# Performance work log

Measured on AMD Instinct MI355X. Metric: run time of the kernel, lower is better.

## Reference

```python
import jax, jax.numpy as jnp
import numpy as np

N = 100000      # num nodes
E = 1600000     # num edges
F_IN = 602      # Reddit input features
H = 256         # num_hidden
C = 42          # num_classes


def gcn_conv(x, src, dst, W, b, num_nodes):
    """PyG GCNConv: add self loops, symmetric deg^-1/2 normalization, scatter-add."""
    h = x @ W  # [N, out] dense transform first (PyG order)
    self_idx = jnp.arange(num_nodes, dtype=src.dtype)
    s = jnp.concatenate([src, self_idx])  # [E+N]
    d = jnp.concatenate([dst, self_idx])
    deg = jax.ops.segment_sum(jnp.ones_like(d, dtype=h.dtype), d, num_segments=num_nodes)
    dinv = deg ** -0.5  # deg >= 1 due to self loops
    norm = dinv[s] * dinv[d]  # [E+N]
    msg = h[s] * norm[:, None]  # [E+N, out] gather + scale
    out = jax.ops.segment_sum(msg, d, num_segments=num_nodes)  # scatter-add
    return out + b


def setup_inputs() -> dict:
    key = jax.random.key(0)
    k = jax.random.split(key, 5)
    x = jax.random.normal(k[0], (N, F_IN), dtype=jnp.float32)
    edge_index = jax.random.randint(k[1], (2, E), 0, N, dtype=jnp.int32)
    # Glorot-style init for GCNConv linear weights; bias zeros (PyG default)
    W1 = jax.random.normal(k[2], (F_IN, H), dtype=jnp.float32) * np.float32(1.0 / np.sqrt(F_IN))
    b1 = jnp.zeros((H,), dtype=jnp.float32)
    W2 = jax.random.normal(k[3], (H, C), dtype=jnp.float32) * np.float32(1.0 / np.sqrt(H))
    b2 = jnp.zeros((C,), dtype=jnp.float32)
    return {"x": x, "edge_index": edge_index, "W1": W1, "b1": b1, "W2": W2, "b2": b2}


def reference(x, edge_index, W1, b1, W2, b2):
    src, dst = edge_index[0], edge_index[1]
    num_nodes = x.shape[0]
    h = gcn_conv(x, src, dst, W1, b1, num_nodes)
    h = jax.nn.relu(h)
    # dropout is identity in eval mode (deterministic reference)
    out = gcn_conv(h, src, dst, W2, b2, num_nodes)
    return jax.nn.log_softmax(out, axis=1)
```

## Files before the change

kernel.cpp:

```cpp
#include <hip/hip_runtime.h>
#include <stdint.h>

#define NN 100000
#define NE 1600000
#define FIN 602
#define KP1 608
#define H 256
#define C 42
#define NP2 48
#define NB1 98

typedef __bf16 bf16;
typedef __bf16 bf16x8 __attribute__((ext_vector_type(8)));
typedef float f32x4 __attribute__((ext_vector_type(4)));

__device__ __forceinline__ float b2f(bf16 v) { return (float)v; }
__device__ __forceinline__ bf16 f2b(float v) { return (bf16)v; }
__device__ __forceinline__ float us2f(unsigned short u) {
    union { unsigned int i; float f; } w; w.i = ((unsigned int)u) << 16; return w.f;
}


__global__ void k_zero(int* __restrict__ p, int n) {
    int i = blockIdx.x * 256 + threadIdx.x;
    if (i < n) p[i] = 0;
}

__global__ void k_count(const int* __restrict__ dst, int* __restrict__ cnt) {
    int e = blockIdx.x * 256 + threadIdx.x;
    if (e < NE) atomicAdd(&cnt[dst[e]], 1);
}

__global__ void k_dinv(const int* __restrict__ cnt, float* __restrict__ dinv) {
    int i = blockIdx.x * 256 + threadIdx.x;
    if (i < NN) dinv[i] = rsqrtf((float)(cnt[i] + 1));
}

__global__ __launch_bounds__(256) void k_scan1(const int* __restrict__ cnt,
                                               int* __restrict__ excl, int* __restrict__ bsum) {
    __shared__ int ts[256];
    const int tid = threadIdx.x;
    const int base = blockIdx.x * 1024 + tid * 4;
    int v[4];
#pragma unroll
    for (int j = 0; j < 4; ++j) v[j] = (base + j < NN) ? cnt[base + j] : 0;
    int s = v[0] + v[1] + v[2] + v[3];
    ts[tid] = s;
    __syncthreads();
    for (int off = 1; off < 256; off <<= 1) {
        int t = (tid >= off) ? ts[tid - off] : 0;
        __syncthreads();
        if (tid >= off) ts[tid] += t;
        __syncthreads();
    }
    int prefix = ts[tid] - s;
    if (tid == 255) bsum[blockIdx.x] = ts[255];
    int run = prefix;
#pragma unroll
    for (int j = 0; j < 4; ++j) {
        if (base + j < NN) excl[base + j] = run;
        run += v[j];
    }
}

__global__ __launch_bounds__(128) void k_scan2(int* __restrict__ bsum) {
    __shared__ int ts[128];
    const int tid = threadIdx.x;
    int v = (tid < NB1) ? bsum[tid] : 0;
    ts[tid] = v;
    __syncthreads();
    for (int off = 1; off < 128; off <<= 1) {
        int t = (tid >= off) ? ts[tid - off] : 0;
        __syncthreads();
        if (tid >= off) ts[tid] += t;
        __syncthreads();
    }
    if (tid < NB1) bsum[tid] = ts[tid] - v;
}

__global__ __launch_bounds__(256) void k_scan3(const int* __restrict__ excl, const int* __restrict__ bsum,
                                               int* __restrict__ rowptr, int* __restrict__ cursor) {
    const int tid = threadIdx.x;
    const int base = blockIdx.x * 1024 + tid * 4;
    const int add = bsum[blockIdx.x];
#pragma unroll
    for (int j = 0; j < 4; ++j) {
        int i = base + j;
        if (i < NN) { int r = excl[i] + add; rowptr[i] = r; cursor[i] = r; }
    }
    if (blockIdx.x == 0 && tid == 0) rowptr[NN] = NE;
}

__global__ void k_fill(const int* __restrict__ src, const int* __restrict__ dst,
                       int* __restrict__ cursor, int* __restrict__ esrc) {
    int e = blockIdx.x * 256 + threadIdx.x;
    if (e < NE) {
        int d = dst[e];
        int pos = atomicAdd(&cursor[d], 1);
        esrc[pos] = src[e];
    }
}


__global__ void k_transpose_w1(const float* __restrict__ w1, bf16* __restrict__ w1t) {
    int idx = blockIdx.x * 256 + threadIdx.x;
    int n = idx / KP1;
    int k = idx % KP1;
    w1t[idx] = (k < FIN) ? f2b(w1[(size_t)k * H + n]) : (bf16)0.0f;
}

__global__ void k_transpose_w2(const float* __restrict__ w2, bf16* __restrict__ w2t) {
    int idx = blockIdx.x * 256 + threadIdx.x;
    int n = idx >> 8;
    int k = idx & 255;
    w2t[idx] = (n < C) ? f2b(w2[(size_t)k * C + n]) : (bf16)0.0f;
}


__global__ __launch_bounds__(256) void k_gemm1(const float* __restrict__ x,
                                               const bf16* __restrict__ w1t,
                                               bf16* __restrict__ h1) {
    const int tid = threadIdx.x;
    const int wave = tid >> 6;
    const int lane = tid & 63;
    const int q = lane >> 4;
    const int r = lane & 15;
    const int b = blockIdx.x;
    const int row0 = (b >> 1) * 64;
    const int col0 = (b & 1) * 128 + wave * 32;

    const float* arow[4];
#pragma unroll
    for (int rt = 0; rt < 4; ++rt) {
        int m = row0 + rt * 16 + r;
        if (m >= NN) m = NN - 1;
        arow[rt] = x + (size_t)m * FIN + q * 8;
    }
    const bf16* brow[2];
#pragma unroll
    for (int ct = 0; ct < 2; ++ct)
        brow[ct] = w1t + (size_t)(col0 + ct * 16 + r) * KP1 + q * 8;

    f32x4 acc[4][2];
#pragma unroll
    for (int a = 0; a < 4; ++a)
#pragma unroll
        for (int c = 0; c < 2; ++c) acc[a][c] = (f32x4){0.f, 0.f, 0.f, 0.f};

#pragma unroll 2
    for (int kk = 0; kk < 18; ++kk) {
        const int k0 = kk * 32;
        bf16x8 af[4];
#pragma unroll
        for (int rt = 0; rt < 4; ++rt) {
            const float2* p = (const float2*)(arow[rt] + k0);
            float2 f0 = p[0], f1 = p[1], f2 = p[2], f3 = p[3];
            union { bf16 s[8]; bf16x8 v; } pk;
            pk.s[0] = f2b(f0.x); pk.s[1] = f2b(f0.y);
            pk.s[2] = f2b(f1.x); pk.s[3] = f2b(f1.y);
            pk.s[4] = f2b(f2.x); pk.s[5] = f2b(f2.y);
            pk.s[6] = f2b(f3.x); pk.s[7] = f2b(f3.y);
            af[rt] = pk.v;
        }
#pragma unroll
        for (int ct = 0; ct < 2; ++ct) {
            union { uint4 u; bf16x8 v; } ub;
            ub.u = *(const uint4*)(brow[ct] + k0);
#pragma unroll
            for (int rt = 0; rt < 4; ++rt)
                acc[rt][ct] = __builtin_amdgcn_mfma_f32_16x16x32_bf16(af[rt], ub.v, acc[rt][ct], 0, 0, 0);
        }
    }

    {
        const int k0 = 576;
        bf16x8 af[4];
#pragma unroll
        for (int rt = 0; rt < 4; ++rt) {
            union { bf16 s[8]; bf16x8 v; } pk;
            if (q < 3) {
                const float2* p = (const float2*)(arow[rt] + k0);
                float2 f0 = p[0], f1 = p[1], f2 = p[2], f3 = p[3];
                pk.s[0] = f2b(f0.x); pk.s[1] = f2b(f0.y);
                pk.s[2] = f2b(f1.x); pk.s[3] = f2b(f1.y);
                pk.s[4] = f2b(f2.x); pk.s[5] = f2b(f2.y);
                pk.s[6] = f2b(f3.x); pk.s[7] = f2b(f3.y);
            } else {
                const float* p = arow[rt] + k0;
                pk.s[0] = f2b(p[0]); pk.s[1] = f2b(p[1]);
#pragma unroll
                for (int j = 2; j < 8; ++j) pk.s[j] = (bf16)0.0f;
            }
            af[rt] = pk.v;
        }
#pragma unroll
        for (int ct = 0; ct < 2; ++ct) {
            union { uint4 u; bf16x8 v; } ub;
            ub.u = *(const uint4*)(brow[ct] + k0);
#pragma unroll
            for (int rt = 0; rt < 4; ++rt)
                acc[rt][ct] = __builtin_amdgcn_mfma_f32_16x16x32_bf16(af[rt], ub.v, acc[rt][ct], 0, 0, 0);
        }
    }

#pragma unroll
    for (int rt = 0; rt < 4; ++rt) {
#pragma unroll
        for (int ct = 0; ct < 2; ++ct) {
            const int col = col0 + ct * 16 + r;
#pragma unroll
            for (int rr = 0; rr < 4; ++rr) {
                const int m = row0 + rt * 16 + q * 4 + rr;
                if (m < NN) h1[(size_t)m * H + col] = f2b(acc[rt][ct][rr]);
            }
        }
    }
}


__global__ __launch_bounds__(64) void k_gather1(const int* __restrict__ rowptr,
                                                const int* __restrict__ esrc,
                                                const bf16* __restrict__ h1,
                                                const float* __restrict__ dinv,
                                                const float* __restrict__ b1,
                                                bf16* __restrict__ hb) {
    const int n = blockIdx.x;
    const int tid = threadIdx.x;
    const float dn = dinv[n];

    uint2 u = ((const uint2*)(h1 + (size_t)n * H))[tid];
    float ws = dn * dn;
    float a0 = us2f((unsigned short)(u.x & 0xffff)) * ws;
    float a1 = us2f((unsigned short)(u.x >> 16)) * ws;
    float a2 = us2f((unsigned short)(u.y & 0xffff)) * ws;
    float a3 = us2f((unsigned short)(u.y >> 16)) * ws;

    const int beg = rowptr[n], end = rowptr[n + 1];
    int j = beg;
    for (; j + 3 < end; j += 4) {
        int s0 = esrc[j], s1 = esrc[j + 1], s2 = esrc[j + 2], s3 = esrc[j + 3];
        float w0 = dinv[s0] * dn, w1 = dinv[s1] * dn, w2 = dinv[s2] * dn, w3 = dinv[s3] * dn;
        uint2 v0 = ((const uint2*)(h1 + (size_t)s0 * H))[tid];
        uint2 v1 = ((const uint2*)(h1 + (size_t)s1 * H))[tid];
        uint2 v2 = ((const uint2*)(h1 + (size_t)s2 * H))[tid];
        uint2 v3 = ((const uint2*)(h1 + (size_t)s3 * H))[tid];
        a0 += us2f((unsigned short)(v0.x & 0xffff)) * w0;
        a1 += us2f((unsigned short)(v0.x >> 16)) * w0;
        a2 += us2f((unsigned short)(v0.y & 0xffff)) * w0;
        a3 += us2f((unsigned short)(v0.y >> 16)) * w0;
        a0 += us2f((unsigned short)(v1.x & 0xffff)) * w1;
        a1 += us2f((unsigned short)(v1.x >> 16)) * w1;
        a2 += us2f((unsigned short)(v1.y & 0xffff)) * w1;
        a3 += us2f((unsigned short)(v1.y >> 16)) * w1;
        a0 += us2f((unsigned short)(v2.x & 0xffff)) * w2;
        a1 += us2f((unsigned short)(v2.x >> 16)) * w2;
        a2 += us2f((unsigned short)(v2.y & 0xffff)) * w2;
        a3 += us2f((unsigned short)(v2.y >> 16)) * w2;
        a0 += us2f((unsigned short)(v3.x & 0xffff)) * w3;
        a1 += us2f((unsigned short)(v3.x >> 16)) * w3;
        a2 += us2f((unsigned short)(v3.y & 0xffff)) * w3;
        a3 += us2f((unsigned short)(v3.y >> 16)) * w3;
    }
    for (; j < end; ++j) {
        int s = esrc[j];
        float w = dinv[s] * dn;
        uint2 v = ((const uint2*)(h1 + (size_t)s * H))[tid];
        a0 += us2f((unsigned short)(v.x & 0xffff)) * w;
        a1 += us2f((unsigned short)(v.x >> 16)) * w;
        a2 += us2f((unsigned short)(v.y & 0xffff)) * w;
        a3 += us2f((unsigned short)(v.y >> 16)) * w;
    }

    float4 bb = ((const float4*)b1)[tid];
    a0 += bb.x; a1 += bb.y; a2 += bb.z; a3 += bb.w;
    a0 = a0 > 0.f ? a0 : 0.f;
    a1 = a1 > 0.f ? a1 : 0.f;
    a2 = a2 > 0.f ? a2 : 0.f;
    a3 = a3 > 0.f ? a3 : 0.f;

    union { unsigned short s[4]; uint2 u; } pk;
    union { bf16 b; unsigned short s; } cv;
    cv.b = f2b(a0); pk.s[0] = cv.s;
    cv.b = f2b(a1); pk.s[1] = cv.s;
    cv.b = f2b(a2); pk.s[2] = cv.s;
    cv.b = f2b(a3); pk.s[3] = cv.s;
    ((uint2*)(hb + (size_t)n * H))[tid] = pk.u;
}


__global__ __launch_bounds__(256) void k_gemm2(const bf16* __restrict__ hb,
                                               const bf16* __restrict__ w2t,
                                               bf16* __restrict__ h2) {
    const int tid = threadIdx.x;
    const int wave = tid >> 6;
    const int lane = tid & 63;
    const int q = lane >> 4;
    const int r = lane & 15;
    const int row0 = blockIdx.x * 128 + wave * 32;

    const bf16* arow[2];
#pragma unroll
    for (int rt = 0; rt < 2; ++rt) {
        int m = row0 + rt * 16 + r;
        if (m >= NN) m = NN - 1;
        arow[rt] = hb + (size_t)m * H + q * 8;
    }
    const bf16* brow[3];
#pragma unroll
    for (int ct = 0; ct < 3; ++ct)
        brow[ct] = w2t + (size_t)(ct * 16 + r) * H + q * 8;

    f32x4 acc[2][3];
#pragma unroll
    for (int a = 0; a < 2; ++a)
#pragma unroll
        for (int c = 0; c < 3; ++c) acc[a][c] = (f32x4){0.f, 0.f, 0.f, 0.f};

#pragma unroll 2
    for (int kk = 0; kk < 8; ++kk) {
        const int k0 = kk * 32;
        bf16x8 af[2];
#pragma unroll
        for (int rt = 0; rt < 2; ++rt) {
            union { uint4 u; bf16x8 v; } ua;
            ua.u = *(const uint4*)(arow[rt] + k0);
            af[rt] = ua.v;
        }
#pragma unroll
        for (int ct = 0; ct < 3; ++ct) {
            union { uint4 u; bf16x8 v; } ub;
            ub.u = *(const uint4*)(brow[ct] + k0);
#pragma unroll
            for (int rt = 0; rt < 2; ++rt)
                acc[rt][ct] = __builtin_amdgcn_mfma_f32_16x16x32_bf16(af[rt], ub.v, acc[rt][ct], 0, 0, 0);
        }
    }

#pragma unroll
    for (int rt = 0; rt < 2; ++rt) {
#pragma unroll
        for (int ct = 0; ct < 3; ++ct) {
            const int col = ct * 16 + r;
            if (col < C) {
#pragma unroll
                for (int rr = 0; rr < 4; ++rr) {
                    const int m = row0 + rt * 16 + q * 4 + rr;
                    if (m < NN) h2[(size_t)m * C + col] = f2b(acc[rt][ct][rr]);
                }
            }
        }
    }
}


__global__ __launch_bounds__(64) void k_gather2(const int* __restrict__ rowptr,
                                                const int* __restrict__ esrc,
                                                const bf16* __restrict__ h2,
                                                const float* __restrict__ dinv,
                                                const float* __restrict__ b2,
                                                float* __restrict__ out) {
    const int n = blockIdx.x;
    const int c = threadIdx.x;
    const float dn = dinv[n];

    float acc = 0.f;
    if (c < C) acc = b2f(h2[(size_t)n * C + c]) * dn * dn;

    const int beg = rowptr[n], end = rowptr[n + 1];
    int j = beg;
    for (; j + 3 < end; j += 4) {
        int s0 = esrc[j], s1 = esrc[j + 1], s2 = esrc[j + 2], s3 = esrc[j + 3];
        float w0 = dinv[s0] * dn, w1 = dinv[s1] * dn, w2 = dinv[s2] * dn, w3 = dinv[s3] * dn;
        if (c < C) {
            float v0 = b2f(h2[(size_t)s0 * C + c]);
            float v1 = b2f(h2[(size_t)s1 * C + c]);
            float v2 = b2f(h2[(size_t)s2 * C + c]);
            float v3 = b2f(h2[(size_t)s3 * C + c]);
            acc += v0 * w0 + v1 * w1 + v2 * w2 + v3 * w3;
        }
    }
    for (; j < end; ++j) {
        int s = esrc[j];
        float w = dinv[s] * dn;
        if (c < C) acc += b2f(h2[(size_t)s * C + c]) * w;
    }

    float v = (c < C) ? acc + b2[c] : -INFINITY;
    float m = v;
#pragma unroll
    for (int o = 32; o > 0; o >>= 1) m = fmaxf(m, __shfl_xor(m, o, 64));
    float ex = (c < C) ? expf(v - m) : 0.f;
    float s = ex;
#pragma unroll
    for (int o = 32; o > 0; o >>= 1) s += __shfl_xor(s, o, 64);
    if (c < C) out[(size_t)n * C + c] = (v - m) - logf(s);
}


extern "C" void kernel_launch(void* const* d_in, const int* in_sizes, int n_in,
                              void* d_out, int out_size, void* d_ws, size_t ws_size,
                              hipStream_t stream) {
    const float* x  = (const float*)d_in[0];
    const int*   ei = (const int*)d_in[1];
    const float* w1 = (const float*)d_in[2];
    const float* b1 = (const float*)d_in[3];
    const float* w2 = (const float*)d_in[4];
    const float* b2 = (const float*)d_in[5];
    float* out = (float*)d_out;

    const int* src = ei;
    const int* dst = ei + NE;

    char* base = (char*)d_ws;
    size_t off = 0;
    auto alloc = [&](size_t bytes) -> void* {
        void* p = base + off;
        off += (bytes + 255) & ~(size_t)255;
        return p;
    };
    int*   cnt    = (int*)alloc((size_t)NN * 4);
    float* dinv   = (float*)alloc((size_t)NN * 4);
    int*   excl   = (int*)alloc((size_t)NN * 4);
    int*   bsum   = (int*)alloc(128 * 4);
    int*   rowptr = (int*)alloc((size_t)(NN + 1) * 4);
    int*   cursor = (int*)alloc((size_t)NN * 4);
    int*   esrc   = (int*)alloc((size_t)NE * 4);
    bf16*  w1t    = (bf16*)alloc((size_t)H * KP1 * 2);
    bf16*  w2t    = (bf16*)alloc((size_t)NP2 * H * 2);
    bf16*  h1     = (bf16*)alloc((size_t)NN * H * 2);
    bf16*  hb     = (bf16*)alloc((size_t)NN * H * 2);
    bf16*  h2     = (bf16*)alloc((size_t)NN * C * 2);
    (void)ws_size;

    k_zero<<<dim3((NN + 255) / 256), dim3(256), 0, stream>>>(cnt, NN);
    k_count<<<dim3((NE + 255) / 256), dim3(256), 0, stream>>>(dst, cnt);
    k_dinv<<<dim3((NN + 255) / 256), dim3(256), 0, stream>>>(cnt, dinv);
    k_scan1<<<dim3(NB1), dim3(256), 0, stream>>>(cnt, excl, bsum);
    k_scan2<<<dim3(1), dim3(128), 0, stream>>>(bsum);
    k_scan3<<<dim3(NB1), dim3(256), 0, stream>>>(excl, bsum, rowptr, cursor);
    k_fill<<<dim3((NE + 255) / 256), dim3(256), 0, stream>>>(src, dst, cursor, esrc);

    k_transpose_w1<<<dim3(KP1), dim3(256), 0, stream>>>(w1, w1t);
    k_transpose_w2<<<dim3(NP2), dim3(256), 0, stream>>>(w2, w2t);

    k_gemm1<<<dim3(2 * ((NN + 63) / 64)), dim3(256), 0, stream>>>(x, w1t, h1);
    k_gather1<<<dim3(NN), dim3(64), 0, stream>>>(rowptr, esrc, h1, dinv, b1, hb);

    k_gemm2<<<dim3((NN + 127) / 128), dim3(256), 0, stream>>>(hb, w2t, h2);
    k_gather2<<<dim3(NN), dim3(64), 0, stream>>>(rowptr, esrc, h2, dinv, b2, out);
}
```

Baseline: 944.3 us.

## Pre-convert x to padded bf16 and pipeline GEMM1 through LDS

A separate kernel first converts the fp32 input features into a padded bf16 buffer. GEMM1 then covers 128 rows by all 256 columns per 512-thread block, streaming A tiles into a triple-buffered, XOR-swizzled LDS ring with direct global-to-LDS loads. Each block now reads x once instead of twice, and the wider per-wave tile means more reuse of each loaded fragment. The cost is an extra pass that writes and re-reads the bf16 copy, and the workspace for hb/h2 is aliased onto the xb buffer.

```diff
diff --git a/kernel.cpp b/kernel.cpp
--- a/kernel.cpp
+++ b/kernel.cpp
@@ -9,6 +9,8 @@
 #define C 42
 #define NP2 48
 #define NB1 98
+#define KBLK 32
+#define NCH (NN * 76)
 
 typedef __bf16 bf16;
 typedef __bf16 bf16x8 __attribute__((ext_vector_type(8)));
@@ -117,100 +119,119 @@
 }
 
 
-__global__ __launch_bounds__(256) void k_gemm1(const float* __restrict__ x,
-                                               const bf16* __restrict__ w1t,
-                                               bf16* __restrict__ h1) {
+__global__ __launch_bounds__(256) void k_convert(const float* __restrict__ x,
+                                                 bf16* __restrict__ xb) {
+    int idx = blockIdx.x * 256 + threadIdx.x;
+    if (idx >= NCH) return;
+    int n = idx / 76;
+    int rem = idx - n * 76;
+    int c0 = rem * 8;
+    const float* p = x + (size_t)n * FIN + c0;
+    union { bf16 s[8]; uint4 u; } pk;
+    if (c0 + 8 <= FIN) {
+        float2 f0 = ((const float2*)p)[0];
+        float2 f1 = ((const float2*)p)[1];
+        float2 f2v = ((const float2*)p)[2];
+        float2 f3 = ((const float2*)p)[3];
+        pk.s[0] = f2b(f0.x);  pk.s[1] = f2b(f0.y);
+        pk.s[2] = f2b(f1.x);  pk.s[3] = f2b(f1.y);
+        pk.s[4] = f2b(f2v.x); pk.s[5] = f2b(f2v.y);
+        pk.s[6] = f2b(f3.x);  pk.s[7] = f2b(f3.y);
+    } else {
+#pragma unroll
+        for (int j = 0; j < 8; ++j)
+            pk.s[j] = (c0 + j < FIN) ? f2b(p[j]) : (bf16)0.0f;
+    }
+    *(uint4*)(xb + (size_t)n * KP1 + c0) = pk.u;
+}
+
+
+__global__ __launch_bounds__(512, 4) void k_gemm1(const bf16* __restrict__ xb,
+                                                  const bf16* __restrict__ w1t,
+                                                  bf16* __restrict__ h1) {
+    __shared__ bf16 As[3 * 128 * KBLK];
     const int tid = threadIdx.x;
     const int wave = tid >> 6;
     const int lane = tid & 63;
     const int q = lane >> 4;
     const int r = lane & 15;
-    const int b = blockIdx.x;
-    const int row0 = (b >> 1) * 64;
-    const int col0 = (b & 1) * 128 + wave * 32;
-
-    const float* arow[4];
+    const int row0 = blockIdx.x * 128;
+    const int wrow0 = (wave & 1) * 64;
+    const int wcol0 = (wave >> 1) * 64;
+
+    const int sg = (tid & 3) ^ ((tid >> 2) & 3) ^ ((tid >> 4) & 3);
+    int gsrow = row0 + (tid >> 2);
+    if (gsrow >= NN) gsrow = NN - 1;
+    const bf16* gsrc = xb + (size_t)gsrow * KP1 + sg * 8;
+
+    int aoff[4];
 #pragma unroll
     for (int rt = 0; rt < 4; ++rt) {
-        int m = row0 + rt * 16 + r;
-        if (m >= NN) m = NN - 1;
-        arow[rt] = x + (size_t)m * FIN + q * 8;
-    }
-    const bf16* brow[2];
-#pragma unroll
-    for (int ct = 0; ct < 2; ++ct)
-        brow[ct] = w1t + (size_t)(col0 + ct * 16 + r) * KP1 + q * 8;
-
-    f32x4 acc[4][2];
+        int R = wrow0 + rt * 16 + r;
+        int gq = q ^ (R & 3) ^ ((R >> 2) & 3);
+        aoff[rt] = R * KBLK + gq * 8;
+    }
+
+    const bf16* brow[4];
+#pragma unroll
+    for (int ct = 0; ct < 4; ++ct)
+        brow[ct] = w1t + (size_t)(wcol0 + ct * 16 + r) * KP1 + q * 8;
+
+    f32x4 acc[4][4];
 #pragma unroll
     for (int a = 0; a < 4; ++a)
 #pragma unroll
-        for (int c = 0; c < 2; ++c) acc[a][c] = (f32x4){0.f, 0.f, 0.f, 0.f};
-
-#pragma unroll 2
-    for (int kk = 0; kk < 18; ++kk) {
-        const int k0 = kk * 32;
+        for (int b = 0; b < 4; ++b) acc[a][b] = (f32x4){0.f, 0.f, 0.f, 0.f};
+
+    auto stage = [&](int bi, int kk) {
+        const bf16* g = gsrc + kk * KBLK;
+        bf16* l = As + bi * (128 * KBLK) + tid * 8;
+        __builtin_amdgcn_global_load_lds(
+            (const __attribute__((address_space(1))) unsigned int*)g,
+            (__attribute__((address_space(3))) unsigned int*)l, 16, 0, 0);
+    };
+
+    stage(0, 0);
+    stage(1, 1);
+    asm volatile("s_waitcnt vmcnt(1)" ::: "memory");
+    __builtin_amdgcn_s_barrier();
+
+    int cur = 0, nx2 = 2;
+#pragma unroll 1
+    for (int kk = 0; kk < 19; ++kk) {
+        const int k0 = kk * KBLK;
+        union { uint4 u; bf16x8 v; } ub[4];
+#pragma unroll
+        for (int ct = 0; ct < 4; ++ct) ub[ct].u = *(const uint4*)(brow[ct] + k0);
+        if (kk + 2 < 19) stage(nx2, kk + 2);
+        const bf16* bufk = As + cur * (128 * KBLK);
         bf16x8 af[4];
 #pragma unroll
         for (int rt = 0; rt < 4; ++rt) {
-            const float2* p = (const float2*)(arow[rt] + k0);
-            float2 f0 = p[0], f1 = p[1], f2 = p[2], f3 = p[3];
-            union { bf16 s[8]; bf16x8 v; } pk;
-            pk.s[0] = f2b(f0.x); pk.s[1] = f2b(f0.y);
-            pk.s[2] = f2b(f1.x); pk.s[3] = f2b(f1.y);
-            pk.s[4] = f2b(f2.x); pk.s[5] = f2b(f2.y);
-            pk.s[6] = f2b(f3.x); pk.s[7] = f2b(f3.y);
-            af[rt] = pk.v;
-        }
-#pragma unroll
-        for (int ct = 0; ct < 2; ++ct) {
-            union { uint4 u; bf16x8 v; } ub;
-            ub.u = *(const uint4*)(brow[ct] + k0);
+            union { uint4 u; bf16x8 v; } ua;
+            ua.u = *(const uint4*)(bufk + aoff[rt]);
+            af[rt] = ua.v;
+        }
+#pragma unroll
+        for (int ct = 0; ct < 4; ++ct)
 #pragma unroll
             for (int rt = 0; rt < 4; ++rt)
-                acc[rt][ct] = __builtin_amdgcn_mfma_f32_16x16x32_bf16(af[rt], ub.v, acc[rt][ct], 0, 0, 0);
-        }
-    }
-
-    {
-        const int k0 = 576;
-        bf16x8 af[4];
-#pragma unroll
-        for (int rt = 0; rt < 4; ++rt) {
-            union { bf16 s[8]; bf16x8 v; } pk;
-            if (q < 3) {
-                const float2* p = (const float2*)(arow[rt] + k0);
-                float2 f0 = p[0], f1 = p[1], f2 = p[2], f3 = p[3];
-                pk.s[0] = f2b(f0.x); pk.s[1] = f2b(f0.y);
-                pk.s[2] = f2b(f1.x); pk.s[3] = f2b(f1.y);
-                pk.s[4] = f2b(f2.x); pk.s[5] = f2b(f2.y);
-                pk.s[6] = f2b(f3.x); pk.s[7] = f2b(f3.y);
-            } else {
-                const float* p = arow[rt] + k0;
-                pk.s[0] = f2b(p[0]); pk.s[1] = f2b(p[1]);
-#pragma unroll
-                for (int j = 2; j < 8; ++j) pk.s[j] = (bf16)0.0f;
-            }
-            af[rt] = pk.v;
-        }
-#pragma unroll
-        for (int ct = 0; ct < 2; ++ct) {
-            union { uint4 u; bf16x8 v; } ub;
-            ub.u = *(const uint4*)(brow[ct] + k0);
-#pragma unroll
-            for (int rt = 0; rt < 4; ++rt)
-                acc[rt][ct] = __builtin_amdgcn_mfma_f32_16x16x32_bf16(af[rt], ub.v, acc[rt][ct], 0, 0, 0);
-        }
+                acc[rt][ct] = __builtin_amdgcn_mfma_f32_16x16x32_bf16(af[rt], ub[ct].v, acc[rt][ct], 0, 0, 0);
+        if (kk + 2 < 19) asm volatile("s_waitcnt vmcnt(1)" ::: "memory");
+        else             asm volatile("s_waitcnt vmcnt(0)" ::: "memory");
+        __builtin_amdgcn_s_barrier();
+        cur = (cur == 2) ? 0 : cur + 1;
+        nx2 = (nx2 == 2) ? 0 : nx2 + 1;
     }
 
 #pragma unroll
     for (int rt = 0; rt < 4; ++rt) {
 #pragma unroll
-        for (int ct = 0; ct < 2; ++ct) {
-            const int col = col0 + ct * 16 + r;
+        for (int ct = 0; ct < 4; ++ct) {
+            const int col = wcol0 + ct * 16 + r;
 #pragma unroll
             for (int rr = 0; rr < 4; ++rr) {
-                const int m = row0 + rt * 16 + q * 4 + rr;
+                const int m = row0 + wrow0 + rt * 16 + q * 4 + rr;
                 if (m < NN) h1[(size_t)m * H + col] = f2b(acc[rt][ct][rr]);
             }
         }
@@ -428,8 +449,9 @@
     bf16*  w1t    = (bf16*)alloc((size_t)H * KP1 * 2);
     bf16*  w2t    = (bf16*)alloc((size_t)NP2 * H * 2);
     bf16*  h1     = (bf16*)alloc((size_t)NN * H * 2);
-    bf16*  hb     = (bf16*)alloc((size_t)NN * H * 2);
-    bf16*  h2     = (bf16*)alloc((size_t)NN * C * 2);
+    bf16*  xb     = (bf16*)alloc((size_t)NN * KP1 * 2);
+    bf16*  hb     = xb;
+    bf16*  h2     = xb + (size_t)NN * H;
     (void)ws_size;
 
     k_zero<<<dim3((NN + 255) / 256), dim3(256), 0, stream>>>(cnt, NN);
@@ -443,7 +465,8 @@
     k_transpose_w1<<<dim3(KP1), dim3(256), 0, stream>>>(w1, w1t);
     k_transpose_w2<<<dim3(NP2), dim3(256), 0, stream>>>(w2, w2t);
 
-    k_gemm1<<<dim3(2 * ((NN + 63) / 64)), dim3(256), 0, stream>>>(x, w1t, h1);
+    k_convert<<<dim3((NCH + 255) / 256), dim3(256), 0, stream>>>(x, xb);
+    k_gemm1<<<dim3((NN + 127) / 128), dim3(512), 0, stream>>>(xb, w1t, h1);
     k_gather1<<<dim3(NN), dim3(64), 0, stream>>>(rowptr, esrc, h1, dinv, b1, hb);
 
     k_gemm2<<<dim3((NN + 127) / 128), dim3(256), 0, stream>>>(hb, w2t, h2);
```

Result: faster. 830.5 us (-12.1%).
